# Optimization experiments

Hardware: AMD Instinct MI355X
Metric: run time of the kernel (lower is better)

## Reference

```python
import jax, jax.numpy as jnp
import numpy as np

T, B, D = 64, 256, 2000
TN, E, H, A, V = 3000, 256, 256, 128, 128
PS, PE, S = 64, 64, 128
G1N, G1L, G2N, G2L = 1500, 4, 1500, 6


def setup_inputs():
    key = jax.random.key(0)
    ks = jax.random.split(key, 32)
    def nrm(k, shape, s=0.05):
        return jax.random.normal(k, shape, dtype=jnp.float32) * s
    inp = {}
    inp["X"] = jax.random.uniform(ks[0], (T, B, D), dtype=jnp.float32)
    inp["profiles"] = nrm(ks[1], (B, PS), 1.0)
    inp["ini_embd"] = nrm(ks[2], (TN, E), 1.0)
    inp["Wa_w"] = nrm(ks[3], (2 * E, A))
    inp["Wa_b"] = jnp.zeros((A,), jnp.float32)
    inp["Ua_w"] = nrm(ks[4], (A, 1))
    inp["gru_Wih"] = nrm(ks[5], (3 * H, E))
    inp["gru_Whh"] = nrm(ks[6], (3 * H, H))
    inp["gru_bih"] = jnp.zeros((3 * H,), jnp.float32)
    inp["gru_bhh"] = jnp.zeros((3 * H,), jnp.float32)
    inp["tranH_w"] = nrm(ks[7], (H + PE, E))
    inp["tranH_b"] = jnp.zeros((E,), jnp.float32)
    inp["out_w"] = nrm(ks[8], (H + V + PE, D))
    inp["out_b"] = jnp.zeros((D,), jnp.float32)
    inp["erase_w"] = nrm(ks[9], (E, V))
    inp["erase_b"] = jnp.zeros((V,), jnp.float32)
    inp["add_w"] = nrm(ks[10], (E, V))
    inp["add_b"] = jnp.zeros((V,), jnp.float32)
    inp["iniVam"] = nrm(ks[11], (S, V), 1.0)
    inp["emP_w"] = nrm(ks[12], (PS, PE))
    inp["emP_b"] = jnp.zeros((PE,), jnp.float32)
    inp["attnP_w"] = nrm(ks[13], (PE + V, PE))
    inp["attnP_b"] = jnp.zeros((PE,), jnp.float32)
    inp["KMIds"] = jax.random.randint(ks[14], (S,), 0, TN, dtype=jnp.int32)
    inp["leaves1"] = jax.random.randint(ks[15], (G1N, G1L), 0, TN, dtype=jnp.int32)
    inp["anc1"] = jax.random.randint(ks[16], (G1N, G1L), 0, TN, dtype=jnp.int32)
    inp["leaves2"] = jax.random.randint(ks[17], (G2N, G2L), 0, TN, dtype=jnp.int32)
    inp["anc2"] = jax.random.randint(ks[18], (G2N, G2L), 0, TN, dtype=jnp.int32)
    inp["mapInfo"] = jax.random.randint(ks[19], (D,), 0, G1N + G2N, dtype=jnp.int32)
    lens = jnp.sort(jax.random.randint(ks[20], (B,), 1, T + 1, dtype=jnp.int32))[::-1]
    inp["X_lengths"] = lens.at[0].set(T)
    return inp


def _forward(floats, ints):
    (X, profiles, ini_embd, Wa_w, Wa_b, Ua_w, gru_Wih, gru_Whh, gru_bih, gru_bhh,
     tranH_w, tranH_b, out_w, out_b, erase_w, erase_b, add_w, add_b, iniVam,
     emP_w, emP_b, attnP_w, attnP_b) = floats
    KMIds, leaves1, anc1, leaves2, anc2, mapInfo, X_lengths = ints

    # GRAM-style ontology attention over (leaf, ancestor) pairs, grouped by path length
    def group_embed(leaves, anc):
        le = ini_embd[leaves]                                     # [N,L,E]
        ae = ini_embd[anc]                                        # [N,L,E]
        hdn = jnp.tanh(jnp.concatenate([le, ae], axis=2) @ Wa_w + Wa_b)
        w = jax.nn.softmax(hdn @ Ua_w, axis=1)                    # [N,L,1]
        return jnp.sum(w * ae, axis=1)                            # [N,E]

    embedMat = jnp.concatenate([group_embed(leaves1, anc1),
                                group_embed(leaves2, anc2)], axis=0)[mapInfo]  # [D,E]
    Xe = jnp.einsum('tbd,de->tbe', X, embedMat)                   # [T,B,E]

    # packed-sequence GRU: frozen state / zero output beyond each sample's length
    mask = (jnp.arange(T)[:, None] < X_lengths[None, :])[..., None]  # [T,B,1]

    def gru_step(h, tup):
        x_t, m_t = tup
        gx = x_t @ gru_Wih.T + gru_bih
        gh = h @ gru_Whh.T + gru_bhh
        r = jax.nn.sigmoid(gx[:, :H] + gh[:, :H])
        z = jax.nn.sigmoid(gx[:, H:2 * H] + gh[:, H:2 * H])
        n = jnp.tanh(gx[:, 2 * H:] + r * gh[:, 2 * H:])
        h_new = (1.0 - z) * n + z * h
        h = jnp.where(m_t, h_new, h)
        return h, jnp.where(m_t, h, 0.0)

    h0 = jnp.zeros((B, H), jnp.float32)
    _, gru_out = jax.lax.scan(gru_step, h0, (Xe, mask))           # [T,B,H]

    prof = profiles @ emP_w + emP_b                               # [B,PE]
    prof_rep = jnp.broadcast_to(prof[None], (T, B, PE))
    tran = jnp.concatenate([gru_out, prof_rep], axis=2) @ tranH_w + tranH_b  # [T,B,E]
    KM = ini_embd[KMIds]                                          # [S,E]
    slot_w = jax.nn.softmax(jnp.einsum('tbe,se->tbs', tran, KM), axis=2)     # [T,B,S]

    # erase/add gates depend only on Xe -> precompute, then scan VM recurrence
    erase = jax.nn.sigmoid(Xe @ erase_w + erase_b)                # [T,B,V]
    add = jnp.tanh(Xe @ add_w + add_b)                            # [T,B,V]

    def mem_step(VM, tup):
        sw, er, ad = tup                                          # [B,S],[B,V],[B,V]
        read = jnp.einsum('bs,bsv->bv', sw, VM)
        VM = VM * (1.0 - sw[:, :, None] * er[:, None, :]) + sw[:, :, None] * ad[:, None, :]
        return VM, read

    VM0 = jnp.broadcast_to(iniVam[None], (B, S, V))
    _, read = jax.lax.scan(mem_step, VM0, (slot_w, erase, add))   # read: [T,B,V]

    attn = jax.nn.relu(jnp.concatenate([prof_rep, read], axis=2) @ attnP_w + attnP_b)
    prof2 = prof_rep * attn
    final = jnp.concatenate([gru_out, read, prof2], axis=2)       # [T,B,H+V+PE]
    # dropout is identity (eval / drop_rate=0)
    return jax.nn.softmax(final @ out_w + out_b, axis=2)          # [T,B,D]


def reference(X, profiles, ini_embd, Wa_w, Wa_b, Ua_w, gru_Wih, gru_Whh, gru_bih, gru_bhh, tranH_w, tranH_b, out_w, out_b, erase_w, erase_b, add_w, add_b, iniVam, emP_w, emP_b, attnP_w, attnP_b, KMIds, leaves1, anc1, leaves2, anc2, mapInfo, X_lengths):
    floats = (X, profiles, ini_embd, Wa_w, Wa_b, Ua_w, gru_Wih, gru_Whh, gru_bih, gru_bhh,
              tranH_w, tranH_b, out_w, out_b, erase_w, erase_b, add_w, add_b, iniVam,
              emP_w, emP_b, attnP_w, attnP_b)
    ints = (KMIds, leaves1, anc1, leaves2, anc2, mapInfo, X_lengths)
    return _forward(floats, ints)
```

## Files before the change

kernel.cpp:

```cpp
#include <hip/hip_runtime.h>
#include <hip/hip_bf16.h>
#include <cmath>

#define T_  64
#define B_  256
#define D_  2000
#define TN_ 3000
#define E_  256
#define H_  256
#define A_  128
#define V_  128
#define PS_ 64
#define PE_ 64
#define S_  128
#define G1N_ 1500
#define G1L_ 4
#define G2N_ 1500
#define G2L_ 6
#define M_  (T_ * B_)
#define KF_ (H_ + V_ + PE_)
#define NREG 28
#define SK_ 4

typedef __attribute__((ext_vector_type(8))) short short8_t;
typedef __attribute__((ext_vector_type(4))) float floatx4;
typedef _Float16 __attribute__((ext_vector_type(2))) h2_t;
typedef _Float16 __attribute__((ext_vector_type(8))) h8_t;

static __device__ __forceinline__ float sigmoidf_(float x) {
    return 1.0f / (1.0f + __expf(-x));
}

static __device__ __forceinline__ void bsplit_(float v, __hip_bfloat16& hi, __hip_bfloat16& lo) {
    hi = __float2bfloat16(v);
    lo = __float2bfloat16(v - __bfloat162float(hi));
}

static __device__ __forceinline__ float dot2_(unsigned int w, unsigned int h, float acc) {
    union { unsigned int u; h2_t h; } cw, ch;
    cw.u = w; ch.u = h;
#if __has_builtin(__builtin_amdgcn_fdot2)
    return __builtin_amdgcn_fdot2(cw.h, ch.h, acc, false);
#else
    return acc + (float)cw.h[0] * (float)ch.h[0] + (float)cw.h[1] * (float)ch.h[1];
#endif
}

template<int DT>
static __device__ __forceinline__ floatx4 mfma16_(short8_t a, short8_t b, floatx4 c) {
    if constexpr (DT == 0) {
        return __builtin_amdgcn_mfma_f32_16x16x32_bf16(a, b, c, 0, 0, 0);
    } else {
        union { short8_t s; h8_t h; } ua, ub;
        ua.s = a; ub.s = b;
        return __builtin_amdgcn_mfma_f32_16x16x32_f16(ua.h, ub.h, c, 0, 0, 0);
    }
}

template<int EPI, bool ACCUM, int OUTMODE, int NPH, int DT>
__global__ __launch_bounds__(256)
void k_mgemm3(const __hip_bfloat16* __restrict__ Ahi, const __hip_bfloat16* __restrict__ Alo,
              const __hip_bfloat16* __restrict__ Bhi, const __hip_bfloat16* __restrict__ Blo,
              const float* __restrict__ bias, float* __restrict__ Cf,
              __hip_bfloat16* __restrict__ Chi, __hip_bfloat16* __restrict__ Clo,
              int K, int Nreal, int nblk)
{
    __shared__ __align__(16) short As[4096];
    __shared__ __align__(16) short Bs[4096];

    const int tid  = threadIdx.x;
    const int lane = tid & 63;
    const int w    = tid >> 6;
    const int wm   = w >> 1, wn = w & 1;
    const int lr   = lane & 15;
    const int lkc  = lane >> 4;

    const int bx = blockIdx.x;
    const int m0 = (bx / nblk) * 128;
    const int n0 = (bx % nblk) * 128;

    const int fa = 2 * w;
    const size_t aoff0 = (size_t)(m0 + fa * 16 + lr) * K + lkc * 8;
    const size_t aoff1 = aoff0 + (size_t)16 * K;
    const size_t boff0 = (size_t)(n0 + fa * 16 + lr) * K + lkc * 8;
    const size_t boff1 = boff0 + (size_t)16 * K;

    floatx4 acc[4][4];
#pragma unroll
    for (int i = 0; i < 4; ++i)
#pragma unroll
        for (int j = 0; j < 4; ++j) acc[i][j] = floatx4{0.f, 0.f, 0.f, 0.f};

#pragma unroll 1
    for (int ph = 0; ph < NPH; ++ph) {
        const __hip_bfloat16* Ap = (ph == 2) ? Alo : Ahi;
        const __hip_bfloat16* Bp = (ph == 1) ? Blo : Bhi;

        short8_t ra0 = *(const short8_t*)(const void*)(Ap + aoff0);
        short8_t ra1 = *(const short8_t*)(const void*)(Ap + aoff1);
        short8_t rb0 = *(const short8_t*)(const void*)(Bp + boff0);
        short8_t rb1 = *(const short8_t*)(const void*)(Bp + boff1);

        for (int k0 = 0; k0 < K; k0 += 32) {
            __syncthreads();
            *(short8_t*)(void*)&As[(fa    ) * 512 + lane * 8] = ra0;
            *(short8_t*)(void*)&As[(fa + 1) * 512 + lane * 8] = ra1;
            *(short8_t*)(void*)&Bs[(fa    ) * 512 + lane * 8] = rb0;
            *(short8_t*)(void*)&Bs[(fa + 1) * 512 + lane * 8] = rb1;
            __syncthreads();

            if (k0 + 32 < K) {
                int kn = k0 + 32;
                ra0 = *(const short8_t*)(const void*)(Ap + aoff0 + kn);
                ra1 = *(const short8_t*)(const void*)(Ap + aoff1 + kn);
                rb0 = *(const short8_t*)(const void*)(Bp + boff0 + kn);
                rb1 = *(const short8_t*)(const void*)(Bp + boff1 + kn);
            }

            short8_t af[4], bf[4];
#pragma unroll
            for (int i = 0; i < 4; ++i)
                af[i] = *(const short8_t*)(const void*)&As[(wm * 4 + i) * 512 + lane * 8];
#pragma unroll
            for (int j = 0; j < 4; ++j)
                bf[j] = *(const short8_t*)(const void*)&Bs[(wn * 4 + j) * 512 + lane * 8];
#pragma unroll
            for (int i = 0; i < 4; ++i)
#pragma unroll
                for (int j = 0; j < 4; ++j)
                    acc[i][j] = mfma16_<DT>(af[i], bf[j], acc[i][j]);
        }
    }

#pragma unroll
    for (int i = 0; i < 4; ++i) {
        const int row = m0 + wm * 64 + i * 16 + (lane >> 4) * 4;
#pragma unroll
        for (int j = 0; j < 4; ++j) {
            const int col = n0 + wn * 64 + j * 16 + (lane & 15);
            if (col < Nreal) {
                float bv = bias ? bias[col] : 0.0f;
#pragma unroll
                for (int r = 0; r < 4; ++r) {
                    float v = acc[i][j][r] + bv;
                    if (EPI == 1) v = (col < 128) ? sigmoidf_(v) : tanhf(v);
                    if (EPI == 2) {
                        if (col < 128) v = sigmoidf_(v);
                        else if (col < 256) v = tanhf(v);
                    }
                    size_t o = (size_t)(row + r) * Nreal + col;
                    if (OUTMODE == 0) {
                        if (ACCUM) v += Cf[o];
                        Cf[o] = v;
                    } else {
                        __hip_bfloat16 h, l;
                        bsplit_(v, h, l);
                        Chi[o] = h; Clo[o] = l;
                    }
                }
            }
        }
    }
}

__global__ __launch_bounds__(256)
void k_mgemmX(const float* __restrict__ A,
              const __hip_bfloat16* __restrict__ Bhi, const __hip_bfloat16* __restrict__ Blo,
              float* __restrict__ P4)
{
    const int KP = 2048, KR = 2000, NN = 256, nblk = 2;
    const int KC = 2048 / SK_;
    __shared__ __align__(16) short Ah[4096];
    __shared__ __align__(16) short Al[4096];
    __shared__ __align__(16) short Bh[4096];
    __shared__ __align__(16) short Bl[4096];

    const int tid  = threadIdx.x;
    const int lane = tid & 63;
    const int w    = tid >> 6;
    const int wm   = w >> 1, wn = w & 1;
    const int lr   = lane & 15;
    const int lkc  = lane >> 4;

    const int kc = blockIdx.x >> 8;
    const int bx = blockIdx.x & 255;
    const int m0 = (bx / nblk) * 128;
    const int n0 = (bx % nblk) * 128;
    const int KC0 = kc * KC;
    float* dst = P4 + (size_t)kc * (M_ * 256);

    const int fa = 2 * w;
    const float* arow0 = A + (size_t)(m0 + fa * 16 + lr) * KR;
    const float* arow1 = arow0 + (size_t)16 * KR;
    const size_t boff0 = (size_t)(n0 + fa * 16 + lr) * KP + lkc * 8;
    const size_t boff1 = boff0 + (size_t)16 * KP;

    floatx4 acc[4][4];
#pragma unroll
    for (int i = 0; i < 4; ++i)
#pragma unroll
        for (int j = 0; j < 4; ++j) acc[i][j] = floatx4{0.f, 0.f, 0.f, 0.f};

    float a0v[8], a1v[8];
    short8_t bh0, bh1, bl0, bl1;

#define LOADA8(ROW, KB, DST)                                                  \
    if ((KB) + 7 < KR) {                                                      \
        float4 p_ = *(const float4*)((ROW) + (KB));                           \
        float4 q_ = *(const float4*)((ROW) + (KB) + 4);                       \
        DST[0]=p_.x; DST[1]=p_.y; DST[2]=p_.z; DST[3]=p_.w;                   \
        DST[4]=q_.x; DST[5]=q_.y; DST[6]=q_.z; DST[7]=q_.w;                   \
    } else {                                                                  \
        _Pragma("unroll")                                                     \
        for (int ii = 0; ii < 8; ++ii)                                        \
            DST[ii] = ((KB) + ii < KR) ? (ROW)[(KB) + ii] : 0.0f;             \
    }

    {
        const int kb = KC0 + lkc * 8;
        LOADA8(arow0, kb, a0v)
        LOADA8(arow1, kb, a1v)
        bh0 = *(const short8_t*)(const void*)(Bhi + boff0 + KC0);
        bh1 = *(const short8_t*)(const void*)(Bhi + boff1 + KC0);
        bl0 = *(const short8_t*)(const void*)(Blo + boff0 + KC0);
        bl1 = *(const short8_t*)(const void*)(Blo + boff1 + KC0);
    }

    for (int k0 = KC0; k0 < KC0 + KC; k0 += 32) {
        __syncthreads();
        {
            short h8a[8], l8a[8], h8b[8], l8b[8];
#pragma unroll
            for (int i = 0; i < 8; ++i) {
                __hip_bfloat16 h, l;
                bsplit_(a0v[i], h, l);
                h8a[i] = *(short*)&h; l8a[i] = *(short*)&l;
                bsplit_(a1v[i], h, l);
                h8b[i] = *(short*)&h; l8b[i] = *(short*)&l;
            }
            *(short8_t*)(void*)&Ah[(fa    ) * 512 + lane * 8] = *(short8_t*)h8a;
            *(short8_t*)(void*)&Al[(fa    ) * 512 + lane * 8] = *(short8_t*)l8a;
            *(short8_t*)(void*)&Ah[(fa + 1) * 512 + lane * 8] = *(short8_t*)h8b;
            *(short8_t*)(void*)&Al[(fa + 1) * 512 + lane * 8] = *(short8_t*)l8b;
            *(short8_t*)(void*)&Bh[(fa    ) * 512 + lane * 8] = bh0;
            *(short8_t*)(void*)&Bh[(fa + 1) * 512 + lane * 8] = bh1;
            *(short8_t*)(void*)&Bl[(fa    ) * 512 + lane * 8] = bl0;
            *(short8_t*)(void*)&Bl[(fa + 1) * 512 + lane * 8] = bl1;
        }
        __syncthreads();

        if (k0 + 32 < KC0 + KC) {
            const int kb = k0 + 32 + lkc * 8;
            LOADA8(arow0, kb, a0v)
            LOADA8(arow1, kb, a1v)
            bh0 = *(const short8_t*)(const void*)(Bhi + boff0 + k0 + 32);
            bh1 = *(const short8_t*)(const void*)(Bhi + boff1 + k0 + 32);
            bl0 = *(const short8_t*)(const void*)(Blo + boff0 + k0 + 32);
            bl1 = *(const short8_t*)(const void*)(Blo + boff1 + k0 + 32);
        }

        short8_t afh[4], afl[4], bfh[4], bfl[4];
#pragma unroll
        for (int i = 0; i < 4; ++i) {
            afh[i] = *(const short8_t*)(const void*)&Ah[(wm * 4 + i) * 512 + lane * 8];
            bfh[i] = *(const short8_t*)(const void*)&Bh[(wn * 4 + i) * 512 + lane * 8];
        }
#pragma unroll
        for (int i = 0; i < 4; ++i)
#pragma unroll
            for (int j = 0; j < 4; ++j)
                acc[i][j] = mfma16_<0>(afh[i], bfh[j], acc[i][j]);
#pragma unroll
        for (int j = 0; j < 4; ++j)
            bfl[j] = *(const short8_t*)(const void*)&Bl[(wn * 4 + j) * 512 + lane * 8];
#pragma unroll
        for (int i = 0; i < 4; ++i)
#pragma unroll
            for (int j = 0; j < 4; ++j)
                acc[i][j] = mfma16_<0>(afh[i], bfl[j], acc[i][j]);
#pragma unroll
        for (int i = 0; i < 4; ++i)
            afl[i] = *(const short8_t*)(const void*)&Al[(wm * 4 + i) * 512 + lane * 8];
#pragma unroll
        for (int i = 0; i < 4; ++i)
#pragma unroll
            for (int j = 0; j < 4; ++j)
                acc[i][j] = mfma16_<0>(afl[i], bfh[j], acc[i][j]);
    }
#undef LOADA8

#pragma unroll
    for (int i = 0; i < 4; ++i) {
        const int row = m0 + wm * 64 + i * 16 + (lane >> 4) * 4;
#pragma unroll
        for (int j = 0; j < 4; ++j) {
            const int col = n0 + wn * 64 + j * 16 + (lane & 15);
#pragma unroll
            for (int r = 0; r < 4; ++r)
                dst[(size_t)(row + r) * NN + col] = acc[i][j][r];
        }
    }
}

__global__ void k_reduceX(const float* __restrict__ P4,
                          __hip_bfloat16* __restrict__ hi, __hip_bfloat16* __restrict__ lo)
{
    int idx = blockIdx.x * blockDim.x + threadIdx.x;
    if (idx >= M_ * 256) return;
    const size_t CH = (size_t)M_ * 256;
    float v = P4[idx];
#pragma unroll
    for (int c = 1; c < SK_; ++c) v += P4[idx + c * CH];
    bsplit_(v, hi[idx], lo[idx]);
}

template<int BM, int BN, int BK, int TM, int TN>
__global__ __launch_bounds__(256)
void k_gemm(const float* __restrict__ A, const float* __restrict__ B,
            float* __restrict__ C, int M, int N, int K)
{
    __shared__ float As[BK][BM + 4];
    __shared__ float Bs[BK][BN + 4];
    const int tid = threadIdx.y * blockDim.x + threadIdx.x;
    const int m0 = blockIdx.y * BM;
    const int n0 = blockIdx.x * BN;
    float acc[TM][TN];
#pragma unroll
    for (int i = 0; i < TM; ++i)
#pragma unroll
        for (int j = 0; j < TN; ++j) acc[i][j] = 0.0f;
    for (int k0 = 0; k0 < K; k0 += BK) {
#pragma unroll
        for (int i = tid; i < BM * BK; i += 256) {
            int r = i / BK, c = i % BK;
            int m = m0 + r;
            As[c][r] = (m < M) ? A[(size_t)m * K + k0 + c] : 0.0f;
        }
#pragma unroll
        for (int i = tid; i < BK * BN; i += 256) {
            int r = i / BN, c = i % BN;
            Bs[r][c] = B[(size_t)(k0 + r) * N + n0 + c];
        }
        __syncthreads();
#pragma unroll
        for (int kk = 0; kk < BK; ++kk) {
            float a[TM], b[TN];
#pragma unroll
            for (int i = 0; i < TM; ++i) a[i] = As[kk][threadIdx.y * TM + i];
#pragma unroll
            for (int j = 0; j < TN; ++j) b[j] = Bs[kk][threadIdx.x * TN + j];
#pragma unroll
            for (int i = 0; i < TM; ++i)
#pragma unroll
                for (int j = 0; j < TN; ++j) acc[i][j] += a[i] * b[j];
        }
        __syncthreads();
    }
#pragma unroll
    for (int i = 0; i < TM; ++i) {
        int m = m0 + threadIdx.y * TM + i;
        if (m >= M) continue;
#pragma unroll
        for (int j = 0; j < TN; ++j)
            C[(size_t)m * N + n0 + threadIdx.x * TN + j] = acc[i][j];
    }
}

__global__ void k_pack_w2(const float* __restrict__ Wa_w, float* __restrict__ W2)
{
    int idx = blockIdx.x * blockDim.x + threadIdx.x;
    if (idx >= E_ * 2 * A_) return;
    int e = idx / (2 * A_), j = idx % (2 * A_);
    W2[idx] = (j < A_) ? Wa_w[(size_t)e * A_ + j]
                       : Wa_w[(size_t)(E_ + e) * A_ + (j - A_)];
}

__global__ void k_wg_split(const float* __restrict__ erase_w, const float* __restrict__ add_w,
                           const float* __restrict__ Wih,
                           const float* __restrict__ erase_b, const float* __restrict__ add_b,
                           const float* __restrict__ bih,
                           __hip_bfloat16* __restrict__ WGhi, __hip_bfloat16* __restrict__ WGlo,
                           float* __restrict__ biasG)
{
    int idx = blockIdx.x * blockDim.x + threadIdx.x;
    if (idx < 1024 * 256) {
        int n = idx >> 8, k = idx & 255;
        float v;
        if (n < 128)      v = erase_w[(size_t)k * V_ + n];
        else if (n < 256) v = add_w[(size_t)k * V_ + (n - 128)];
        else              v = Wih[(size_t)(n - 256) * 256 + k];
        bsplit_(v, WGhi[idx], WGlo[idx]);
    }
    if (idx < 1024)
        biasG[idx] = (idx < 128) ? erase_b[idx]
                   : (idx < 256) ? add_b[idx - 128]
                                 : bih[idx - 256];
}

__global__ void k_tranHT_split(const float* __restrict__ tranH_w,
                               __hip_bfloat16* __restrict__ hi, __hip_bfloat16* __restrict__ lo)
{
    int idx = blockIdx.x * blockDim.x + threadIdx.x;
    if (idx >= 256 * 320) return;
    int n = idx / 320, k = idx % 320;
    bsplit_(tranH_w[(size_t)k * 256 + n], hi[idx], lo[idx]);
}

__global__ void k_outWT_f16(const float* __restrict__ out_w, _Float16* __restrict__ dst)
{
    int idx = blockIdx.x * blockDim.x + threadIdx.x;
    if (idx >= 2048 * 448) return;
    int n = idx / 448, k = idx % 448;
    float v = (n < D_) ? out_w[(size_t)k * D_ + n] : 0.0f;
    dst[idx] = (_Float16)v;
}

__global__ void k_km_split(const float* __restrict__ ini_embd, const int* __restrict__ KMIds,
                           __hip_bfloat16* __restrict__ hi, __hip_bfloat16* __restrict__ lo)
{
    int idx = blockIdx.x * blockDim.x + threadIdx.x;
    if (idx >= S_ * E_) return;
    int s = idx / E_, k = idx % E_;
    bsplit_(ini_embd[(size_t)KMIds[s] * E_ + k], hi[idx], lo[idx]);
}

__global__ void k_embMT(const float* __restrict__ embG, const int* __restrict__ mapInfo,
                        __hip_bfloat16* __restrict__ hi, __hip_bfloat16* __restrict__ lo)
{
    int idx = blockIdx.x * blockDim.x + threadIdx.x;
    if (idx >= 256 * 2048) return;
    int e = idx >> 11, d = idx & 2047;
    float v = (d < D_) ? embG[(size_t)mapInfo[d] * E_ + e] : 0.0f;
    bsplit_(v, hi[idx], lo[idx]);
}

__global__ void k_wgru_pack(const float* __restrict__ Whh,
                            unsigned int* __restrict__ Wrg, unsigned int* __restrict__ Wst)
{
    int idx = blockIdx.x * blockDim.x + threadIdx.x;
    if (idx >= 768 * 128) return;
    int j = idx / 128, e2 = idx % 128;
    union { unsigned int u; h2_t h; } c;
    c.h[0] = (_Float16)Whh[(size_t)j * 256 + 2 * e2];
    c.h[1] = (_Float16)Whh[(size_t)j * 256 + 2 * e2 + 1];
    if (e2 < 4 * NREG) {
        Wrg[(size_t)e2 * 768 + j] = c.u;
    } else {
        int ee = e2 - 4 * NREG;
        Wst[((size_t)(ee >> 2) * 768 + j) * 4 + (ee & 3)] = c.u;
    }
}

__global__ void k_prof(const float* __restrict__ profiles, const float* __restrict__ emP_w,
                       const float* __restrict__ emP_b, float* __restrict__ prof)
{
    int b = blockIdx.x, j = threadIdx.x;
    float acc = emP_b[j];
    for (int k = 0; k < PS_; ++k) acc += profiles[(size_t)b * PS_ + k] * emP_w[(size_t)k * PE_ + j];
    prof[(size_t)b * PE_ + j] = acc;
}

__global__ void k_fill_tp(const float* __restrict__ prof,
                          __hip_bfloat16* __restrict__ At_hi, __hip_bfloat16* __restrict__ At_lo)
{
    int idx = blockIdx.x * blockDim.x + threadIdx.x;
    if (idx >= M_ * PE_) return;
    int m = idx >> 6, pe = idx & 63;
    float v = prof[(size_t)(m & (B_ - 1)) * PE_ + pe];
    size_t o = (size_t)m * 320 + 256 + pe;
    bsplit_(v, At_hi[o], At_lo[o]);
}

__global__ void k_group_embed(const float* __restrict__ PP, const float* __restrict__ Wa_b,
                              const float* __restrict__ Ua_w, const float* __restrict__ ini_embd,
                              const int* __restrict__ leaves1, const int* __restrict__ anc1,
                              const int* __restrict__ leaves2, const int* __restrict__ anc2,
                              float* __restrict__ embedG)
{
    int n = blockIdx.x;
    int lane = threadIdx.x;
    const int* lv; const int* ac; int L;
    if (n < G1N_) { L = G1L_; lv = leaves1 + (size_t)n * G1L_; ac = anc1 + (size_t)n * G1L_; }
    else { int n2 = n - G1N_; L = G2L_; lv = leaves2 + (size_t)n2 * G2L_; ac = anc2 + (size_t)n2 * G2L_; }

    float score[6]; int ai[6];
    for (int l = 0; l < L; ++l) {
        int li = lv[l]; int av = ac[l]; ai[l] = av;
        float s = 0.0f;
        for (int a = lane; a < A_; a += 64) {
            float hv = tanhf(PP[(size_t)li * 256 + a] + PP[(size_t)av * 256 + 128 + a] + Wa_b[a]);
            s += hv * Ua_w[a];
        }
        for (int o = 32; o; o >>= 1) s += __shfl_xor(s, o);
        score[l] = s;
    }
    float mx = -1e30f;
    for (int l = 0; l < L; ++l) mx = fmaxf(mx, score[l]);
    float w[6], sum = 0.0f;
    for (int l = 0; l < L; ++l) { w[l] = __expf(score[l] - mx); sum += w[l]; }
    float inv = 1.0f / sum;
    for (int e = lane; e < E_; e += 64) {
        float acc = 0.0f;
        for (int l = 0; l < L; ++l) acc += w[l] * inv * ini_embd[(size_t)ai[l] * E_ + e];
        embedG[(size_t)n * E_ + e] = acc;
    }
}

__global__ __launch_bounds__(768, 3)
void k_gru5(const float* __restrict__ Cg, const unsigned int* __restrict__ Wrg,
            const uint4* __restrict__ Wst, const float* __restrict__ bhh,
            const int* __restrict__ X_len, float* __restrict__ gruo,
            __hip_bfloat16* __restrict__ At_hi, __hip_bfloat16* __restrict__ At_lo)
{
    const int b = blockIdx.x;
    const int tid = threadIdx.x;

    __shared__ uint4 h2S[32];
    __shared__ float ghS[768];
    __shared__ float gxnS[256];

    if (tid < 128) ((unsigned int*)h2S)[tid] = 0u;

    uint4 Wr[NREG];
#pragma unroll
    for (int c = 0; c < NREG; ++c) {
        Wr[c].x = Wrg[(size_t)(4 * c + 0) * 768 + tid];
        Wr[c].y = Wrg[(size_t)(4 * c + 1) * 768 + tid];
        Wr[c].z = Wrg[(size_t)(4 * c + 2) * 768 + tid];
        Wr[c].w = Wrg[(size_t)(4 * c + 3) * 768 + tid];
    }

    float hreg = 0.0f;
    const int len = X_len[b];
    const float bj = bhh[tid];
    __syncthreads();

    for (int t = 0; t < T_; ++t) {
        float gxv = Cg[((size_t)t * B_ + b) * 1024 + 256 + tid];

        float a0 = bj;
#pragma unroll
        for (int c = 0; c < 32; ++c) {
            uint4 w = (c < NREG) ? Wr[c] : Wst[(size_t)(c - NREG) * 768 + tid];
            uint4 h = h2S[c];
            a0 = dot2_(w.x, h.x, a0);
            a0 = dot2_(w.y, h.y, a0);
            a0 = dot2_(w.z, h.z, a0);
            a0 = dot2_(w.w, h.w, a0);
        }

        if (tid < 512) ghS[tid] = a0 + gxv;
        else { ghS[tid] = a0; gxnS[tid - 512] = gxv; }
        __syncthreads();

        if (tid < 256) {
            float r  = sigmoidf_(ghS[tid]);
            float z  = sigmoidf_(ghS[256 + tid]);
            float nn = tanhf(gxnS[tid] + r * ghS[512 + tid]);
            float hnew = (1.0f - z) * nn + z * hreg;
            bool msk = (t < len);
            hreg = msk ? hnew : hreg;
            float ov = msk ? hreg : 0.0f;
            size_t m = (size_t)t * B_ + b;
            gruo[m * H_ + tid] = ov;
            size_t o = m * 320 + tid;
            bsplit_(ov, At_hi[o], At_lo[o]);
            float partner = __shfl_xor(hreg, 1);
            if (!(tid & 1)) {
                union { unsigned int u; h2_t h; } p;
                p.h[0] = (_Float16)hreg;
                p.h[1] = (_Float16)partner;
                ((unsigned int*)h2S)[tid >> 1] = p.u;
            }
        }
        __syncthreads();
    }
}

__global__ __launch_bounds__(256)
void k_mem(const float* __restrict__ slotw, const float* __restrict__ Cg,
           const float* __restrict__ iniVam, float* __restrict__ readv)
{
    const int b = blockIdx.x;
    const int tid = threadIdx.x;
    const int v = tid & (V_ - 1);
    const int sh = tid >> 7;
    const int sbase = sh * 64;

    float VM[64];
#pragma unroll
    for (int i = 0; i < 64; ++i) VM[i] = iniVam[(size_t)(sbase + i) * V_ + v];

    __shared__ float swL[S_];
    __shared__ float eaL[2 * V_];
    __shared__ float part[V_];

    for (int t = 0; t < T_; ++t) {
        size_t m = (size_t)t * B_ + b;
        if (tid < S_) swL[tid] = slotw[m * S_ + tid];
        eaL[tid] = Cg[m * 1024 + tid];
        __syncthreads();

        float er = eaL[v], ad = eaL[V_ + v];
        float p0 = 0.0f, p1 = 0.0f, p2 = 0.0f, p3 = 0.0f;
#pragma unroll
        for (int i = 0; i < 16; ++i) {
            float s0 = swL[sbase + 4 * i];
            float s1 = swL[sbase + 4 * i + 1];
            float s2 = swL[sbase + 4 * i + 2];
            float s3 = swL[sbase + 4 * i + 3];
            float v0 = VM[4 * i], v1 = VM[4 * i + 1], v2 = VM[4 * i + 2], v3 = VM[4 * i + 3];
            p0 += s0 * v0; p1 += s1 * v1; p2 += s2 * v2; p3 += s3 * v3;
            VM[4 * i]     = v0 * (1.0f - s0 * er) + s0 * ad;
            VM[4 * i + 1] = v1 * (1.0f - s1 * er) + s1 * ad;
            VM[4 * i + 2] = v2 * (1.0f - s2 * er) + s2 * ad;
            VM[4 * i + 3] = v3 * (1.0f - s3 * er) + s3 * ad;
        }
        float acc = (p0 + p1) + (p2 + p3);
        if (sh == 1) part[v] = acc;
        __syncthreads();
        if (sh == 0) readv[m * V_ + v] = acc + part[v];
        __syncthreads();
    }
}

__global__ __launch_bounds__(256)
void k_build_final(const float* __restrict__ gruo, const float* __restrict__ readv,
                   const float* __restrict__ prof, const float* __restrict__ attnP_w,
                   const float* __restrict__ attnP_b, _Float16* __restrict__ F)
{
    const int m = blockIdx.x;
    const int b = m & (B_ - 1);
    const int tid = threadIdx.x;
    __shared__ float rd[V_];
    __shared__ float pf[PE_];
    if (tid < V_) rd[tid] = readv[(size_t)m * V_ + tid];
    if (tid < PE_) pf[tid] = prof[(size_t)b * PE_ + tid];
    __syncthreads();

    size_t base = (size_t)m * KF_;
    F[base + tid] = (_Float16)gruo[(size_t)m * H_ + tid];
    if (tid < V_) F[base + H_ + tid] = (_Float16)rd[tid];
    if (tid < PE_) {
        float a = attnP_b[tid];
        for (int k = 0; k < PE_; ++k) a += pf[k] * attnP_w[(size_t)k * PE_ + tid];
        for (int k = 0; k < V_; ++k) a += rd[k] * attnP_w[(size_t)(PE_ + k) * PE_ + tid];
        a = fmaxf(a, 0.0f);
        F[base + H_ + V_ + tid] = (_Float16)(pf[tid] * a);
    }
}

__global__ void k_softmax128(float* __restrict__ C)
{
    const int m = blockIdx.x;
    const size_t base = (size_t)m * S_;
    const int lane = threadIdx.x;
    float a = C[base + lane], b = C[base + 64 + lane];
    float mx = fmaxf(a, b);
    for (int o = 32; o; o >>= 1) mx = fmaxf(mx, __shfl_xor(mx, o));
    float e0 = __expf(a - mx), e1 = __expf(b - mx);
    float s = e0 + e1;
    for (int o = 32; o; o >>= 1) s += __shfl_xor(s, o);
    float inv = 1.0f / s;
    C[base + lane] = e0 * inv;
    C[base + 64 + lane] = e1 * inv;
}

__global__ __launch_bounds__(256)
void k_softmax2000(float* __restrict__ C)
{
    const int m = blockIdx.x;
    const size_t base = (size_t)m * D_;
    const int tid = threadIdx.x;
    const int wid = tid >> 6, lane = tid & 63;
    __shared__ float red[4], red2[4];

    float v[8];
#pragma unroll
    for (int i = 0; i < 8; ++i) {
        int d = i * 256 + tid;
        v[i] = (d < D_) ? C[base + d] : -1e30f;
    }
    float mx = v[0];
#pragma unroll
    for (int i = 1; i < 8; ++i) mx = fmaxf(mx, v[i]);
    for (int o = 32; o; o >>= 1) mx = fmaxf(mx, __shfl_xor(mx, o));
    if (lane == 0) red[wid] = mx;
    __syncthreads();
    mx = fmaxf(fmaxf(red[0], red[1]), fmaxf(red[2], red[3]));

    float sum = 0.0f;
#pragma unroll
    for (int i = 0; i < 8; ++i) { v[i] = __expf(v[i] - mx); sum += v[i]; }
    for (int o = 32; o; o >>= 1) sum += __shfl_xor(sum, o);
    if (lane == 0) red2[wid] = sum;
    __syncthreads();
    sum = red2[0] + red2[1] + red2[2] + red2[3];
    float inv = 1.0f / sum;
#pragma unroll
    for (int i = 0; i < 8; ++i) {
        int d = i * 256 + tid;
        if (d < D_) C[base + d] = v[i] * inv;
    }
}

extern "C" void kernel_launch(void* const* d_in, const int* in_sizes, int n_in,
                              void* d_out, int out_size, void* d_ws, size_t ws_size,
                              hipStream_t stream)
{
    const float* X        = (const float*)d_in[0];
    const float* profiles = (const float*)d_in[1];
    const float* ini_embd = (const float*)d_in[2];
    const float* Wa_w     = (const float*)d_in[3];
    const float* Wa_b     = (const float*)d_in[4];
    const float* Ua_w     = (const float*)d_in[5];
    const float* gru_Wih  = (const float*)d_in[6];
    const float* gru_Whh  = (const float*)d_in[7];
    const float* gru_bih  = (const float*)d_in[8];
    const float* gru_bhh  = (const float*)d_in[9];
    const float* tranH_w  = (const float*)d_in[10];
    const float* tranH_b  = (const float*)d_in[11];
    const float* out_w    = (const float*)d_in[12];
    const float* out_b    = (const float*)d_in[13];
    const float* erase_w  = (const float*)d_in[14];
    const float* erase_b  = (const float*)d_in[15];
    const float* add_w    = (const float*)d_in[16];
    const float* add_b    = (const float*)d_in[17];
    const float* iniVam   = (const float*)d_in[18];
    const float* emP_w    = (const float*)d_in[19];
    const float* emP_b    = (const float*)d_in[20];
    const float* attnP_w  = (const float*)d_in[21];
    const float* attnP_b  = (const float*)d_in[22];
    const int* KMIds   = (const int*)d_in[23];
    const int* leaves1 = (const int*)d_in[24];
    const int* anc1    = (const int*)d_in[25];
    const int* leaves2 = (const int*)d_in[26];
    const int* anc2    = (const int*)d_in[27];
    const int* mapInfo = (const int*)d_in[28];
    const int* X_len   = (const int*)d_in[29];

    char* ws = (char*)d_ws;
    float* out = (float*)d_out;
    typedef __hip_bfloat16 bf16;

    const size_t R0 = 0;
    const size_t R1 = 67108864;
    const size_t R2 = 83886080;
    const size_t R3 = 100663296;
    size_t P = 121634816;
    const size_t EMBHI = P; P += 1048576;
    const size_t EMBLO = P; P += 1048576;
    const size_t OWF  = P; P += 1835008;
    const size_t WGHI = P; P += 524288;
    const size_t WGLO = P; P += 524288;
    const size_t THHI = P; P += 163840;
    const size_t THLO = P; P += 163840;
    const size_t KMHI = P; P += 65536;
    const size_t KMLO = P; P += 65536;
    const size_t WRG  = P; P += 344064;
    const size_t WST  = P; P += 49152;
    const size_t PROF = P; P += 65536;
    const size_t BIAS = P; P += 4096;
    const size_t W2O  = P; P += 262144;

    float* PP      = (float*)(ws + R0);
    float* embG    = (float*)(ws + R0 + 12288000);
    float* P4      = (float*)(ws + R0);
    float* Cg      = (float*)(ws + R0);
    _Float16* F16  = (_Float16*)(ws + R0);
    float* gruo    = (float*)(ws + R1);
    bf16*  Xe_hi   = (bf16*)(ws + R2);
    bf16*  Xe_lo   = (bf16*)(ws + R2 + 8388608);
    bf16*  tran_hi = (bf16*)(ws + R2);
    bf16*  tran_lo = (bf16*)(ws + R2 + 8388608);
    bf16*  At_hi   = (bf16*)(ws + R3);
    bf16*  At_lo   = (bf16*)(ws + R3 + 10485760);
    float* slotw   = (float*)(ws + R3);
    float* readv   = (float*)(ws + R3 + 10485760);
    bf16*  EMBhi = (bf16*)(ws + EMBHI); bf16* EMBlo = (bf16*)(ws + EMBLO);
    _Float16* OWf = (_Float16*)(ws + OWF);
    bf16*  WGhi = (bf16*)(ws + WGHI); bf16* WGlo = (bf16*)(ws + WGLO);
    bf16*  THhi = (bf16*)(ws + THHI); bf16* THlo = (bf16*)(ws + THLO);
    bf16*  KMhi = (bf16*)(ws + KMHI); bf16* KMlo = (bf16*)(ws + KMLO);
    unsigned int* Wrg = (unsigned int*)(ws + WRG);
    unsigned int* Wst = (unsigned int*)(ws + WST);
    float* prof  = (float*)(ws + PROF);
    float* biasG = (float*)(ws + BIAS);
    float* W2p   = (float*)(ws + W2O);

    k_pack_w2<<<(E_ * 2 * A_ + 255) / 256, 256, 0, stream>>>(Wa_w, W2p);
    k_wg_split<<<(1024 * 256 + 255) / 256, 256, 0, stream>>>(
        erase_w, add_w, gru_Wih, erase_b, add_b, gru_bih, WGhi, WGlo, biasG);
    k_tranHT_split<<<(256 * 320 + 255) / 256, 256, 0, stream>>>(tranH_w, THhi, THlo);
    k_outWT_f16<<<(2048 * 448 + 255) / 256, 256, 0, stream>>>(out_w, OWf);
    k_km_split<<<(S_ * E_ + 255) / 256, 256, 0, stream>>>(ini_embd, KMIds, KMhi, KMlo);
    k_wgru_pack<<<(768 * 128 + 255) / 256, 256, 0, stream>>>(gru_Whh, Wrg, Wst);
    k_prof<<<B_, PE_, 0, stream>>>(profiles, emP_w, emP_b, prof);

    {
        dim3 blk(16, 16);
        dim3 grid(4, (TN_ + 63) / 64);
        k_gemm<64, 64, 16, 4, 4><<<grid, blk, 0, stream>>>(ini_embd, W2p, PP, TN_, 256, E_);
    }
    k_group_embed<<<G1N_ + G2N_, 64, 0, stream>>>(PP, Wa_b, Ua_w, ini_embd,
                                                  leaves1, anc1, leaves2, anc2, embG);
    k_embMT<<<(256 * 2048) / 256, 256, 0, stream>>>(embG, mapInfo, EMBhi, EMBlo);

    k_mgemmX<<<SK_ * 256, 256, 0, stream>>>(X, EMBhi, EMBlo, P4);
    k_reduceX<<<(M_ * 256) / 256, 256, 0, stream>>>(P4, Xe_hi, Xe_lo);

    k_mgemm3<2, false, 0, 3, 0><<<128 * 8, 256, 0, stream>>>(Xe_hi, Xe_lo, WGhi, WGlo,
        biasG, Cg, nullptr, nullptr, 256, 1024, 8);

    k_gru5<<<256, 768, 0, stream>>>(Cg, Wrg, (const uint4*)Wst, gru_bhh, X_len,
                                    gruo, At_hi, At_lo);
    k_fill_tp<<<(M_ * PE_) / 256, 256, 0, stream>>>(prof, At_hi, At_lo);

    k_mgemm3<0, false, 1, 3, 0><<<128 * 2, 256, 0, stream>>>(At_hi, At_lo, THhi, THlo,
        tranH_b, nullptr, tran_hi, tran_lo, 320, 256, 2);

    k_mgemm3<0, false, 0, 3, 0><<<128 * 1, 256, 0, stream>>>(tran_hi, tran_lo, KMhi, KMlo,
        nullptr, slotw, nullptr, nullptr, 256, 128, 1);

    k_softmax128<<<M_, 64, 0, stream>>>(slotw);
    k_mem<<<B_, 256, 0, stream>>>(slotw, Cg, iniVam, readv);
    k_build_final<<<M_, 256, 0, stream>>>(gruo, readv, prof, attnP_w, attnP_b, F16);

    k_mgemm3<0, false, 0, 1, 1><<<128 * 16, 256, 0, stream>>>(
        (const bf16*)F16, nullptr, (const bf16*)OWf, nullptr,
        out_b, out, nullptr, nullptr, 448, 2000, 16);

    k_softmax2000<<<M_, 256, 0, stream>>>(out);
}
```

Before: 666.7 us.

## Use fp16 two-term split for X-embedding GEMM and fp16 logits buffer

The X×embedding GEMM now converts X to a single fp16 term and splits only the embedding matrix into fp16 hi/lo parts. This drops one of the three bf16 MFMA passes and the A-lo shared memory tile. The output projection now writes fp16 logits to a scratch buffer, and the softmax reads them back, halving the intermediate write/read traffic. X values in [0,1) lose some mantissa precision under fp16, and the fp16 logits also reduce accuracy, so tolerance is a risk.

```diff
diff --git a/kernel.cpp b/kernel.cpp
--- a/kernel.cpp
+++ b/kernel.cpp
@@ -152,10 +152,12 @@
                     if (OUTMODE == 0) {
                         if (ACCUM) v += Cf[o];
                         Cf[o] = v;
-                    } else {
+                    } else if (OUTMODE == 1) {
                         __hip_bfloat16 h, l;
                         bsplit_(v, h, l);
                         Chi[o] = h; Clo[o] = l;
+                    } else {
+                        ((_Float16*)Chi)[o] = (_Float16)v;
                     }
                 }
             }
@@ -165,13 +167,12 @@
 
 __global__ __launch_bounds__(256)
 void k_mgemmX(const float* __restrict__ A,
-              const __hip_bfloat16* __restrict__ Bhi, const __hip_bfloat16* __restrict__ Blo,
+              const _Float16* __restrict__ Bhi, const _Float16* __restrict__ Blo,
               float* __restrict__ P4)
 {
     const int KP = 2048, KR = 2000, NN = 256, nblk = 2;
     const int KC = 2048 / SK_;
     __shared__ __align__(16) short Ah[4096];
-    __shared__ __align__(16) short Al[4096];
     __shared__ __align__(16) short Bh[4096];
     __shared__ __align__(16) short Bl[4096];
 
@@ -229,19 +230,16 @@
     for (int k0 = KC0; k0 < KC0 + KC; k0 += 32) {
         __syncthreads();
         {
-            short h8a[8], l8a[8], h8b[8], l8b[8];
+            short h8a[8], h8b[8];
 #pragma unroll
             for (int i = 0; i < 8; ++i) {
-                __hip_bfloat16 h, l;
-                bsplit_(a0v[i], h, l);
-                h8a[i] = *(short*)&h; l8a[i] = *(short*)&l;
-                bsplit_(a1v[i], h, l);
-                h8b[i] = *(short*)&h; l8b[i] = *(short*)&l;
+                union { _Float16 h; short s; } ca, cb;
+                ca.h = (_Float16)a0v[i];
+                cb.h = (_Float16)a1v[i];
+                h8a[i] = ca.s; h8b[i] = cb.s;
             }
             *(short8_t*)(void*)&Ah[(fa    ) * 512 + lane * 8] = *(short8_t*)h8a;
-            *(short8_t*)(void*)&Al[(fa    ) * 512 + lane * 8] = *(short8_t*)l8a;
             *(short8_t*)(void*)&Ah[(fa + 1) * 512 + lane * 8] = *(short8_t*)h8b;
-            *(short8_t*)(void*)&Al[(fa + 1) * 512 + lane * 8] = *(short8_t*)l8b;
             *(short8_t*)(void*)&Bh[(fa    ) * 512 + lane * 8] = bh0;
             *(short8_t*)(void*)&Bh[(fa + 1) * 512 + lane * 8] = bh1;
             *(short8_t*)(void*)&Bl[(fa    ) * 512 + lane * 8] = bl0;
@@ -259,17 +257,17 @@
             bl1 = *(const short8_t*)(const void*)(Blo + boff1 + k0 + 32);
         }
 
-        short8_t afh[4], afl[4], bfh[4], bfl[4];
+        short8_t af[4], bfh[4], bfl[4];
 #pragma unroll
         for (int i = 0; i < 4; ++i) {
-            afh[i] = *(const short8_t*)(const void*)&Ah[(wm * 4 + i) * 512 + lane * 8];
+            af[i]  = *(const short8_t*)(const void*)&Ah[(wm * 4 + i) * 512 + lane * 8];
             bfh[i] = *(const short8_t*)(const void*)&Bh[(wn * 4 + i) * 512 + lane * 8];
         }
 #pragma unroll
         for (int i = 0; i < 4; ++i)
 #pragma unroll
             for (int j = 0; j < 4; ++j)
-                acc[i][j] = mfma16_<0>(afh[i], bfh[j], acc[i][j]);
+                acc[i][j] = mfma16_<1>(af[i], bfh[j], acc[i][j]);
 #pragma unroll
         for (int j = 0; j < 4; ++j)
             bfl[j] = *(const short8_t*)(const void*)&Bl[(wn * 4 + j) * 512 + lane * 8];
@@ -277,15 +275,7 @@
         for (int i = 0; i < 4; ++i)
 #pragma unroll
             for (int j = 0; j < 4; ++j)
-                acc[i][j] = mfma16_<0>(afh[i], bfl[j], acc[i][j]);
-#pragma unroll
-        for (int i = 0; i < 4; ++i)
-            afl[i] = *(const short8_t*)(const void*)&Al[(wm * 4 + i) * 512 + lane * 8];
-#pragma unroll
-        for (int i = 0; i < 4; ++i)
-#pragma unroll
-            for (int j = 0; j < 4; ++j)
-                acc[i][j] = mfma16_<0>(afl[i], bfh[j], acc[i][j]);
+                acc[i][j] = mfma16_<1>(af[i], bfl[j], acc[i][j]);
     }
 #undef LOADA8
 
@@ -424,14 +414,16 @@
     bsplit_(ini_embd[(size_t)KMIds[s] * E_ + k], hi[idx], lo[idx]);
 }
 
-__global__ void k_embMT(const float* __restrict__ embG, const int* __restrict__ mapInfo,
-                        __hip_bfloat16* __restrict__ hi, __hip_bfloat16* __restrict__ lo)
+__global__ void k_embMT_f16(const float* __restrict__ embG, const int* __restrict__ mapInfo,
+                            _Float16* __restrict__ hi, _Float16* __restrict__ lo)
 {
     int idx = blockIdx.x * blockDim.x + threadIdx.x;
     if (idx >= 256 * 2048) return;
     int e = idx >> 11, d = idx & 2047;
     float v = (d < D_) ? embG[(size_t)mapInfo[d] * E_ + e] : 0.0f;
-    bsplit_(v, hi[idx], lo[idx]);
+    _Float16 h = (_Float16)v;
+    hi[idx] = h;
+    lo[idx] = (_Float16)(v - (float)h);
 }
 
 __global__ void k_wgru_pack(const float* __restrict__ Whh,
@@ -667,7 +659,7 @@
 }
 
 __global__ __launch_bounds__(256)
-void k_softmax2000(float* __restrict__ C)
+void k_softmax2000(const _Float16* __restrict__ L, float* __restrict__ C)
 {
     const int m = blockIdx.x;
     const size_t base = (size_t)m * D_;
@@ -679,7 +671,7 @@
 #pragma unroll
     for (int i = 0; i < 8; ++i) {
         int d = i * 256 + tid;
-        v[i] = (d < D_) ? C[base + d] : -1e30f;
+        v[i] = (d < D_) ? (float)L[base + d] : -1e30f;
     }
     float mx = v[0];
 #pragma unroll
@@ -768,6 +760,7 @@
     float* P4      = (float*)(ws + R0);
     float* Cg      = (float*)(ws + R0);
     _Float16* F16  = (_Float16*)(ws + R0);
+    _Float16* LG16 = (_Float16*)(ws + 16777216);
     float* gruo    = (float*)(ws + R1);
     bf16*  Xe_hi   = (bf16*)(ws + R2);
     bf16*  Xe_lo   = (bf16*)(ws + R2 + 8388608);
@@ -777,7 +770,8 @@
     bf16*  At_lo   = (bf16*)(ws + R3 + 10485760);
     float* slotw   = (float*)(ws + R3);
     float* readv   = (float*)(ws + R3 + 10485760);
-    bf16*  EMBhi = (bf16*)(ws + EMBHI); bf16* EMBlo = (bf16*)(ws + EMBLO);
+    _Float16* EMBhi = (_Float16*)(ws + EMBHI);
+    _Float16* EMBlo = (_Float16*)(ws + EMBLO);
     _Float16* OWf = (_Float16*)(ws + OWF);
     bf16*  WGhi = (bf16*)(ws + WGHI); bf16* WGlo = (bf16*)(ws + WGLO);
     bf16*  THhi = (bf16*)(ws + THHI); bf16* THlo = (bf16*)(ws + THLO);
@@ -804,7 +798,7 @@
     }
     k_group_embed<<<G1N_ + G2N_, 64, 0, stream>>>(PP, Wa_b, Ua_w, ini_embd,
                                                   leaves1, anc1, leaves2, anc2, embG);
-    k_embMT<<<(256 * 2048) / 256, 256, 0, stream>>>(embG, mapInfo, EMBhi, EMBlo);
+    k_embMT_f16<<<(256 * 2048) / 256, 256, 0, stream>>>(embG, mapInfo, EMBhi, EMBlo);
 
     k_mgemmX<<<SK_ * 256, 256, 0, stream>>>(X, EMBhi, EMBlo, P4);
     k_reduceX<<<(M_ * 256) / 256, 256, 0, stream>>>(P4, Xe_hi, Xe_lo);
@@ -826,9 +820,9 @@
     k_mem<<<B_, 256, 0, stream>>>(slotw, Cg, iniVam, readv);
     k_build_final<<<M_, 256, 0, stream>>>(gruo, readv, prof, attnP_w, attnP_b, F16);
 
-    k_mgemm3<0, false, 0, 1, 1><<<128 * 16, 256, 0, stream>>>(
+    k_mgemm3<0, false, 2, 1, 1><<<128 * 16, 256, 0, stream>>>(
         (const bf16*)F16, nullptr, (const bf16*)OWf, nullptr,
-        out_b, out, nullptr, nullptr, 448, 2000, 16);
-
-    k_softmax2000<<<M_, 256, 0, stream>>>(out);
-}
+        out_b, nullptr, (bf16*)LG16, nullptr, 448, 2000, 16);
+
+    k_softmax2000<<<M_, 256, 0, stream>>>(LG16, out);
+}
```

Measured after the change: 654.6 us. No clear change (-1.8%).
